# Performance work log

Measured on AMD Instinct MI355X. Metric: run time of the kernel, lower is better.

## Reference

```python
import jax, jax.numpy as jnp
import numpy as np

NUM_STREAMS = 4
DIM = 256
SINKHORN_ITERS = 10
SINKHORN_TAU = 0.05


def sinkhorn_log(logits, num_iters=SINKHORN_ITERS, tau=SINKHORN_TAU):
    n = logits.shape[-1]
    z = logits / tau
    log_marginal = -jnp.log(jnp.asarray(float(n), dtype=logits.dtype))

    def body(carry, _):
        u, v = carry
        u = log_marginal - jax.scipy.special.logsumexp(z + v[None, :], axis=1)
        v = log_marginal - jax.scipy.special.logsumexp(z + u[:, None], axis=0)
        return (u, v), None

    u0 = jnp.zeros((n,), dtype=z.dtype)
    v0 = jnp.zeros((n,), dtype=z.dtype)
    (u, v), _ = jax.lax.scan(body, (u0, v0), None, length=num_iters)
    return jnp.exp(z + u[:, None] + v[None, :]) * n


def setup_inputs() -> dict:
    key = jax.random.key(0)
    k_res, k_w = jax.random.split(key)
    B = 65536
    residuals = jax.random.normal(k_res, (B, NUM_STREAMS, DIM), dtype=jnp.float32)
    # h_res_logits: -8 everywhere, 0 on diagonal (as in __init__)
    h_res_logits = jnp.full((NUM_STREAMS, NUM_STREAMS), -8.0, dtype=jnp.float32)
    h_res_logits = h_res_logits.at[jnp.arange(NUM_STREAMS), jnp.arange(NUM_STREAMS)].set(0.0)
    # h_pre_logits: -8 everywhere, 0 at init_residual_index=0
    h_pre_logits = jnp.full((NUM_STREAMS,), -8.0, dtype=jnp.float32).at[0].set(0.0)
    h_post_logits = jnp.zeros((NUM_STREAMS,), dtype=jnp.float32)
    # branch Linear(dim, dim, bias=False): weight (out, in), y = x @ W.T
    bound = 1.0 / np.sqrt(DIM)
    W_branch = jax.random.uniform(k_w, (DIM, DIM), dtype=jnp.float32, minval=-bound, maxval=bound)
    return {
        "residuals": residuals,
        "h_res_logits": h_res_logits,
        "h_pre_logits": h_pre_logits,
        "h_post_logits": h_post_logits,
        "W_branch": W_branch,
    }


def reference(residuals, h_res_logits, h_pre_logits, h_post_logits, W_branch):
    # residuals: (B, S, D)
    h_res = sinkhorn_log(h_res_logits)                     # (S, S) doubly-stochastic * n
    h_pre = jax.nn.softmax(h_pre_logits)                   # (S,)
    h_post = jax.nn.softmax(h_post_logits)                 # (S,)
    residuals_mixed = jnp.einsum('st,bsd->btd', h_res, residuals)
    branch_input = jnp.einsum('s,bsd->bd', h_pre, residuals)
    branch_output = branch_input @ W_branch.T              # (B, D)
    depth_out = jnp.einsum('bd,s->bsd', branch_output, h_post)
    return residuals_mixed + depth_out
```

## Files before the change

kernel.cpp:

```cpp
#include <hip/hip_runtime.h>

#define NSTREAMS 4
#define DIM 256
#define BM 16
#define NTHREADS 512
#define TILES 8

typedef __attribute__((ext_vector_type(8))) short short8;
typedef __attribute__((ext_vector_type(4))) float f32x4;

static __device__ __forceinline__ short f2bf(float x) {
    union { float f; unsigned int u; } c; c.f = x;
    unsigned int u = c.u;
    unsigned int lsb = (u >> 16) & 1u;
    u += 0x7fffu + lsb;
    return (short)(u >> 16);
}
static __device__ __forceinline__ int2 f2bf4(float4 v) {
    unsigned int lo, hi;
    asm("v_cvt_pk_bf16_f32 %0, %1, %2" : "=v"(lo) : "v"(v.x), "v"(v.y));
    asm("v_cvt_pk_bf16_f32 %0, %1, %2" : "=v"(hi) : "v"(v.z), "v"(v.w));
    int2 r; r.x = (int)lo; r.y = (int)hi;
    return r;
}

static __device__ __forceinline__ float rfl(float x) {
    int i = __builtin_amdgcn_readfirstlane(__builtin_bit_cast(int, x));
    return __builtin_bit_cast(float, i);
}

static __device__ __forceinline__ void barrier_lgkm() {
    asm volatile("s_waitcnt lgkmcnt(0)\n\ts_barrier" ::: "memory");
}

static __device__ void compute_h(const float* __restrict__ hres_l,
                                 const float* __restrict__ hpre_l,
                                 const float* __restrict__ hpost_l,
                                 float* h_out) {
    const float inv_tau = 1.0f / 0.05f;
    float z[4][4];
    for (int i = 0; i < 4; ++i)
        for (int j = 0; j < 4; ++j)
            z[i][j] = hres_l[i * 4 + j] * inv_tau;
    float u[4] = {0.f, 0.f, 0.f, 0.f};
    float v[4] = {0.f, 0.f, 0.f, 0.f};
    const float logm = -logf(4.0f);
    for (int it = 0; it < 10; ++it) {
        for (int i = 0; i < 4; ++i) {
            float m = -1e30f;
            for (int j = 0; j < 4; ++j) m = fmaxf(m, z[i][j] + v[j]);
            float ss = 0.f;
            for (int j = 0; j < 4; ++j) ss += expf(z[i][j] + v[j] - m);
            u[i] = logm - (m + logf(ss));
        }
        for (int j = 0; j < 4; ++j) {
            float m = -1e30f;
            for (int i = 0; i < 4; ++i) m = fmaxf(m, z[i][j] + u[i]);
            float ss = 0.f;
            for (int i = 0; i < 4; ++i) ss += expf(z[i][j] + u[i] - m);
            v[j] = logm - (m + logf(ss));
        }
    }
    for (int i = 0; i < 4; ++i)
        for (int j = 0; j < 4; ++j)
            h_out[i * 4 + j] = expf(z[i][j] + u[i] + v[j]) * 4.0f;
    {
        float m = fmaxf(fmaxf(hpre_l[0], hpre_l[1]), fmaxf(hpre_l[2], hpre_l[3]));
        float e0 = expf(hpre_l[0] - m), e1 = expf(hpre_l[1] - m);
        float e2 = expf(hpre_l[2] - m), e3 = expf(hpre_l[3] - m);
        float ss = e0 + e1 + e2 + e3;
        h_out[16] = e0 / ss; h_out[17] = e1 / ss; h_out[18] = e2 / ss; h_out[19] = e3 / ss;
    }
    {
        float m = fmaxf(fmaxf(hpost_l[0], hpost_l[1]), fmaxf(hpost_l[2], hpost_l[3]));
        float e0 = expf(hpost_l[0] - m), e1 = expf(hpost_l[1] - m);
        float e2 = expf(hpost_l[2] - m), e3 = expf(hpost_l[3] - m);
        float ss = e0 + e1 + e2 + e3;
        h_out[20] = e0 / ss; h_out[21] = e1 / ss; h_out[22] = e2 / ss; h_out[23] = e3 / ss;
    }
}

__global__ void prep_h_kernel(const float* __restrict__ hres_l,
                              const float* __restrict__ hpre_l,
                              const float* __restrict__ hpost_l,
                              float* __restrict__ ws) {
    if (threadIdx.x == 0) compute_h(hres_l, hpre_l, hpost_l, ws);
}

__global__ __launch_bounds__(256) void prep_wh_kernel(const float* __restrict__ Wb,
                                                      short* __restrict__ wbf,
                                                      const float* __restrict__ hres_l,
                                                      const float* __restrict__ hpre_l,
                                                      const float* __restrict__ hpost_l,
                                                      float* __restrict__ ws_h) {
    int idx = blockIdx.x * 256 + threadIdx.x;
    float4 v = reinterpret_cast<const float4*>(Wb)[idx];
    reinterpret_cast<int2*>(wbf)[idx] = f2bf4(v);
    if (blockIdx.x == 0 && threadIdx.x == 0)
        compute_h(hres_l, hpre_l, hpost_l, ws_h);
}

template <bool USE_WSW>
__global__ __launch_bounds__(NTHREADS, 2) void fused_kernel(
    const float* __restrict__ res,
    const float* __restrict__ Wb,
    const short* __restrict__ wbf,
    const float* __restrict__ hptr,
    const float* __restrict__ hres_l,
    const float* __restrict__ hpre_l,
    const float* __restrict__ hpost_l,
    float* __restrict__ out)
{
    __shared__ __align__(16) short bi_lds[BM][DIM + 8];
    __shared__ __align__(16) float bo_lds[BM][DIM + 4];
    __shared__ float h_sh[24];

    const int t  = threadIdx.x;
    const int d4 = t & 63;
    const int r0 = t >> 6;
    const int w  = t >> 6;
    const int l  = t & 63;
    const int lr = l & 15;
    const int lk = l >> 4;

    if (hptr) {
        if (t < 24) h_sh[t] = hptr[t];
    } else if (t == 0) {
        compute_h(hres_l, hpre_l, hpost_l, h_sh);
    }
    barrier_lgkm();

    const float hp0 = rfl(h_sh[16]), hp1 = rfl(h_sh[17]);
    const float hp2 = rfl(h_sh[18]), hp3 = rfl(h_sh[19]);
    float hres[4][4];
    #pragma unroll
    for (int s = 0; s < 4; ++s)
        #pragma unroll
        for (int tt = 0; tt < 4; ++tt)
            hres[s][tt] = rfl(h_sh[s * 4 + tt]);
    float hq[4] = {rfl(h_sh[20]), rfl(h_sh[21]), rfl(h_sh[22]), rfl(h_sh[23])};

    const long tile0 = (long)blockIdx.x * TILES;

    float4 cur[2][4];
    #pragma unroll
    for (int it = 0; it < 2; ++it) {
        int r = r0 + it * 8;
        const float4* p = reinterpret_cast<const float4*>(
            res + (tile0 * BM + r) * (NSTREAMS * DIM)) + d4;
        cur[it][0] = p[0];
        cur[it][1] = p[64];
        cur[it][2] = p[128];
        cur[it][3] = p[192];
        float4 bi;
        bi.x = hp0 * cur[it][0].x + hp1 * cur[it][1].x + hp2 * cur[it][2].x + hp3 * cur[it][3].x;
        bi.y = hp0 * cur[it][0].y + hp1 * cur[it][1].y + hp2 * cur[it][2].y + hp3 * cur[it][3].y;
        bi.z = hp0 * cur[it][0].z + hp1 * cur[it][1].z + hp2 * cur[it][2].z + hp3 * cur[it][3].z;
        bi.w = hp0 * cur[it][0].w + hp1 * cur[it][1].w + hp2 * cur[it][2].w + hp3 * cur[it][3].w;
        *reinterpret_cast<int2*>(&bi_lds[r][d4 * 4]) = f2bf4(bi);
    }
    barrier_lgkm();

    for (int ti = 0; ti < TILES; ++ti) {
        f32x4 acc[2] = {f32x4{0.f, 0.f, 0.f, 0.f}, f32x4{0.f, 0.f, 0.f, 0.f}};
        for (int k0 = 0; k0 < DIM; k0 += 32) {
            short8 a = *reinterpret_cast<const short8*>(&bi_lds[lr][k0 + lk * 8]);
            #pragma unroll
            for (int nt = 0; nt < 2; ++nt) {
                int dcol = w * 32 + nt * 16 + lr;
                short8 b;
                if (USE_WSW) {
                    b = *reinterpret_cast<const short8*>(wbf + dcol * DIM + k0 + lk * 8);
                } else {
                    const float4* wp = reinterpret_cast<const float4*>(Wb + dcol * DIM + k0 + lk * 8);
                    float4 wa = wp[0];
                    float4 wb2 = wp[1];
                    b[0] = f2bf(wa.x); b[1] = f2bf(wa.y); b[2] = f2bf(wa.z); b[3] = f2bf(wa.w);
                    b[4] = f2bf(wb2.x); b[5] = f2bf(wb2.y); b[6] = f2bf(wb2.z); b[7] = f2bf(wb2.w);
                }
                acc[nt] = __builtin_amdgcn_mfma_f32_16x16x32_bf16(a, b, acc[nt], 0, 0, 0);
            }
        }

        float4 nx[2][4];
        const bool more = (ti + 1 < TILES);
        if (more) {
            #pragma unroll
            for (int it = 0; it < 2; ++it) {
                int r = r0 + it * 8;
                const float4* p = reinterpret_cast<const float4*>(
                    res + ((tile0 + ti + 1) * BM + r) * (NSTREAMS * DIM)) + d4;
                nx[it][0] = p[0];
                nx[it][1] = p[64];
                nx[it][2] = p[128];
                nx[it][3] = p[192];
            }
        }

        #pragma unroll
        for (int nt = 0; nt < 2; ++nt) {
            int d = w * 32 + nt * 16 + lr;
            #pragma unroll
            for (int j = 0; j < 4; ++j)
                bo_lds[lk * 4 + j][d] = acc[nt][j];
        }
        barrier_lgkm();

        #pragma unroll
        for (int it = 0; it < 2; ++it) {
            int r = r0 + it * 8;
            float4 bo = *reinterpret_cast<const float4*>(&bo_lds[r][d4 * 4]);
            float* obase = out + (((tile0 + ti) * BM + r) * 4) * DIM + d4 * 4;
            #pragma unroll
            for (int tt = 0; tt < 4; ++tt) {
                float4 o;
                o.x = hq[tt] * bo.x + hres[0][tt] * cur[it][0].x + hres[1][tt] * cur[it][1].x
                    + hres[2][tt] * cur[it][2].x + hres[3][tt] * cur[it][3].x;
                o.y = hq[tt] * bo.y + hres[0][tt] * cur[it][0].y + hres[1][tt] * cur[it][1].y
                    + hres[2][tt] * cur[it][2].y + hres[3][tt] * cur[it][3].y;
                o.z = hq[tt] * bo.z + hres[0][tt] * cur[it][0].z + hres[1][tt] * cur[it][1].z
                    + hres[2][tt] * cur[it][2].z + hres[3][tt] * cur[it][3].z;
                o.w = hq[tt] * bo.w + hres[0][tt] * cur[it][0].w + hres[1][tt] * cur[it][1].w
                    + hres[2][tt] * cur[it][2].w + hres[3][tt] * cur[it][3].w;
                *reinterpret_cast<float4*>(obase + tt * DIM) = o;
            }
        }

        if (more) {
            #pragma unroll
            for (int it = 0; it < 2; ++it) {
                int r = r0 + it * 8;
                float4 bi;
                bi.x = hp0 * nx[it][0].x + hp1 * nx[it][1].x + hp2 * nx[it][2].x + hp3 * nx[it][3].x;
                bi.y = hp0 * nx[it][0].y + hp1 * nx[it][1].y + hp2 * nx[it][2].y + hp3 * nx[it][3].y;
                bi.z = hp0 * nx[it][0].z + hp1 * nx[it][1].z + hp2 * nx[it][2].z + hp3 * nx[it][3].z;
                bi.w = hp0 * nx[it][0].w + hp1 * nx[it][1].w + hp2 * nx[it][2].w + hp3 * nx[it][3].w;
                *reinterpret_cast<int2*>(&bi_lds[r][d4 * 4]) = f2bf4(bi);
                #pragma unroll
                for (int s = 0; s < 4; ++s)
                    cur[it][s] = nx[it][s];
            }
        }
        barrier_lgkm();
    }
}

extern "C" void kernel_launch(void* const* d_in, const int* in_sizes, int n_in,
                              void* d_out, int out_size, void* d_ws, size_t ws_size,
                              hipStream_t stream) {
    const float* res     = (const float*)d_in[0];
    const float* hres_l  = (const float*)d_in[1];
    const float* hpre_l  = (const float*)d_in[2];
    const float* hpost_l = (const float*)d_in[3];
    const float* Wb      = (const float*)d_in[4];
    float* out = (float*)d_out;

    const int Btot = in_sizes[0] / (NSTREAMS * DIM);
    const int grid = Btot / (BM * TILES);

    const size_t W_OFF = 256;
    const size_t need_h = 24 * sizeof(float);
    const size_t need_w = W_OFF + (size_t)DIM * DIM * sizeof(short);
    const bool has_h = ws_size >= need_h;
    const bool has_w = ws_size >= need_w;

    float* ws_h = (float*)d_ws;
    short* ws_w = (short*)((char*)d_ws + W_OFF);

    if (has_w) {
        prep_wh_kernel<<<(DIM * DIM / 4) / 256, 256, 0, stream>>>(
            Wb, ws_w, hres_l, hpre_l, hpost_l, ws_h);
        fused_kernel<true><<<grid, NTHREADS, 0, stream>>>(
            res, Wb, ws_w, ws_h, hres_l, hpre_l, hpost_l, out);
    } else if (has_h) {
        prep_h_kernel<<<1, 64, 0, stream>>>(hres_l, hpre_l, hpost_l, ws_h);
        fused_kernel<false><<<grid, NTHREADS, 0, stream>>>(
            res, Wb, nullptr, ws_h, hres_l, hpre_l, hpost_l, out);
    } else {
        fused_kernel<false><<<grid, NTHREADS, 0, stream>>>(
            res, Wb, nullptr, nullptr, hres_l, hpre_l, hpost_l, out);
    }
}
```

Measured before the change: 129.7 us.

## Stage full bf16 weight matrix in swizzled LDS with 1024-thread blocks

The whole 256x256 bf16 branch weight is loaded once per block into an XOR-swizzled LDS buffer, so the MFMA loop no longer reads W from global or L2 on every tile. Blocks grow to 1024 threads (16 waves, one 16-column slice each) and each block now covers 16 tiles, with the next tile's residual prefetch issued before the MFMA loop. The cost is 128KB of LDS and one block per CU, which reduces occupancy. It also puts a 128KB weight load at the start of every block.

```diff
diff --git a/kernel.cpp b/kernel.cpp
--- a/kernel.cpp
+++ b/kernel.cpp
@@ -3,8 +3,8 @@
 #define NSTREAMS 4
 #define DIM 256
 #define BM 16
-#define NTHREADS 512
-#define TILES 8
+#define NTHREADS 1024
+#define TILES 16
 
 typedef __attribute__((ext_vector_type(8))) short short8;
 typedef __attribute__((ext_vector_type(4))) float f32x4;
@@ -101,7 +101,7 @@
 }
 
 template <bool USE_WSW>
-__global__ __launch_bounds__(NTHREADS, 2) void fused_kernel(
+__global__ __launch_bounds__(NTHREADS, 1) void fused_kernel(
     const float* __restrict__ res,
     const float* __restrict__ Wb,
     const short* __restrict__ wbf,
@@ -111,6 +111,7 @@
     const float* __restrict__ hpost_l,
     float* __restrict__ out)
 {
+    __shared__ __align__(16) short W_lds[DIM * DIM];
     __shared__ __align__(16) short bi_lds[BM][DIM + 8];
     __shared__ __align__(16) float bo_lds[BM][DIM + 4];
     __shared__ float h_sh[24];
@@ -122,6 +123,35 @@
     const int l  = t & 63;
     const int lr = l & 15;
     const int lk = l >> 4;
+
+    const long tile0 = (long)blockIdx.x * TILES;
+    float4 cur[4];
+    {
+        const float4* p = reinterpret_cast<const float4*>(
+            res + (tile0 * BM + r0) * (NSTREAMS * DIM)) + d4;
+        cur[0] = p[0];
+        cur[1] = p[64];
+        cur[2] = p[128];
+        cur[3] = p[192];
+    }
+
+    #pragma unroll
+    for (int i = 0; i < 8; ++i) {
+        int c = t * 8 + i;
+        int row = c >> 5;
+        int koff = (c & 31) * 16;
+        int dst = (row << 9) | (koff ^ ((row & 7) << 4));
+        int4 wv;
+        if (USE_WSW) {
+            wv = reinterpret_cast<const int4*>(wbf)[c];
+        } else {
+            const float4* wp = reinterpret_cast<const float4*>(Wb) + c * 2;
+            float4 wa = wp[0], wb2 = wp[1];
+            int2 loq = f2bf4(wa), hiq = f2bf4(wb2);
+            wv.x = loq.x; wv.y = loq.y; wv.z = hiq.x; wv.w = hiq.y;
+        }
+        *reinterpret_cast<int4*>(reinterpret_cast<char*>(W_lds) + dst) = wv;
+    }
 
     if (hptr) {
         if (t < 24) h_sh[t] = hptr[t];
@@ -140,106 +170,77 @@
             hres[s][tt] = rfl(h_sh[s * 4 + tt]);
     float hq[4] = {rfl(h_sh[20]), rfl(h_sh[21]), rfl(h_sh[22]), rfl(h_sh[23])};
 
-    const long tile0 = (long)blockIdx.x * TILES;
-
-    float4 cur[2][4];
-    #pragma unroll
-    for (int it = 0; it < 2; ++it) {
-        int r = r0 + it * 8;
-        const float4* p = reinterpret_cast<const float4*>(
-            res + (tile0 * BM + r) * (NSTREAMS * DIM)) + d4;
-        cur[it][0] = p[0];
-        cur[it][1] = p[64];
-        cur[it][2] = p[128];
-        cur[it][3] = p[192];
+    {
         float4 bi;
-        bi.x = hp0 * cur[it][0].x + hp1 * cur[it][1].x + hp2 * cur[it][2].x + hp3 * cur[it][3].x;
-        bi.y = hp0 * cur[it][0].y + hp1 * cur[it][1].y + hp2 * cur[it][2].y + hp3 * cur[it][3].y;
-        bi.z = hp0 * cur[it][0].z + hp1 * cur[it][1].z + hp2 * cur[it][2].z + hp3 * cur[it][3].z;
-        bi.w = hp0 * cur[it][0].w + hp1 * cur[it][1].w + hp2 * cur[it][2].w + hp3 * cur[it][3].w;
-        *reinterpret_cast<int2*>(&bi_lds[r][d4 * 4]) = f2bf4(bi);
+        bi.x = hp0 * cur[0].x + hp1 * cur[1].x + hp2 * cur[2].x + hp3 * cur[3].x;
+        bi.y = hp0 * cur[0].y + hp1 * cur[1].y + hp2 * cur[2].y + hp3 * cur[3].y;
+        bi.z = hp0 * cur[0].z + hp1 * cur[1].z + hp2 * cur[2].z + hp3 * cur[3].z;
+        bi.w = hp0 * cur[0].w + hp1 * cur[1].w + hp2 * cur[2].w + hp3 * cur[3].w;
+        *reinterpret_cast<int2*>(&bi_lds[r0][d4 * 4]) = f2bf4(bi);
     }
     barrier_lgkm();
 
+    const int dcol = w * 16 + lr;
+    const char* wbase = reinterpret_cast<const char*>(W_lds) + (dcol << 9);
+    const int dswz = (dcol & 7) << 4;
+
     for (int ti = 0; ti < TILES; ++ti) {
-        f32x4 acc[2] = {f32x4{0.f, 0.f, 0.f, 0.f}, f32x4{0.f, 0.f, 0.f, 0.f}};
+        const bool more = (ti + 1 < TILES);
+
+        float4 nx[4];
+        if (more) {
+            const float4* p = reinterpret_cast<const float4*>(
+                res + ((tile0 + ti + 1) * BM + r0) * (NSTREAMS * DIM)) + d4;
+            nx[0] = p[0];
+            nx[1] = p[64];
+            nx[2] = p[128];
+            nx[3] = p[192];
+        }
+        __builtin_amdgcn_sched_barrier(0);
+
+        f32x4 acc = {0.f, 0.f, 0.f, 0.f};
+        #pragma unroll
         for (int k0 = 0; k0 < DIM; k0 += 32) {
             short8 a = *reinterpret_cast<const short8*>(&bi_lds[lr][k0 + lk * 8]);
-            #pragma unroll
-            for (int nt = 0; nt < 2; ++nt) {
-                int dcol = w * 32 + nt * 16 + lr;
-                short8 b;
-                if (USE_WSW) {
-                    b = *reinterpret_cast<const short8*>(wbf + dcol * DIM + k0 + lk * 8);
-                } else {
-                    const float4* wp = reinterpret_cast<const float4*>(Wb + dcol * DIM + k0 + lk * 8);
-                    float4 wa = wp[0];
-                    float4 wb2 = wp[1];
-                    b[0] = f2bf(wa.x); b[1] = f2bf(wa.y); b[2] = f2bf(wa.z); b[3] = f2bf(wa.w);
-                    b[4] = f2bf(wb2.x); b[5] = f2bf(wb2.y); b[6] = f2bf(wb2.z); b[7] = f2bf(wb2.w);
-                }
-                acc[nt] = __builtin_amdgcn_mfma_f32_16x16x32_bf16(a, b, acc[nt], 0, 0, 0);
-            }
-        }
-
-        float4 nx[2][4];
-        const bool more = (ti + 1 < TILES);
-        if (more) {
-            #pragma unroll
-            for (int it = 0; it < 2; ++it) {
-                int r = r0 + it * 8;
-                const float4* p = reinterpret_cast<const float4*>(
-                    res + ((tile0 + ti + 1) * BM + r) * (NSTREAMS * DIM)) + d4;
-                nx[it][0] = p[0];
-                nx[it][1] = p[64];
-                nx[it][2] = p[128];
-                nx[it][3] = p[192];
-            }
+            short8 b = *reinterpret_cast<const short8*>(
+                wbase + ((k0 * 2 + lk * 16) ^ dswz));
+            acc = __builtin_amdgcn_mfma_f32_16x16x32_bf16(a, b, acc, 0, 0, 0);
         }
 
         #pragma unroll
-        for (int nt = 0; nt < 2; ++nt) {
-            int d = w * 32 + nt * 16 + lr;
-            #pragma unroll
-            for (int j = 0; j < 4; ++j)
-                bo_lds[lk * 4 + j][d] = acc[nt][j];
-        }
+        for (int j = 0; j < 4; ++j)
+            bo_lds[lk * 4 + j][dcol] = acc[j];
+
         barrier_lgkm();
 
-        #pragma unroll
-        for (int it = 0; it < 2; ++it) {
-            int r = r0 + it * 8;
-            float4 bo = *reinterpret_cast<const float4*>(&bo_lds[r][d4 * 4]);
-            float* obase = out + (((tile0 + ti) * BM + r) * 4) * DIM + d4 * 4;
+        {
+            float4 bo = *reinterpret_cast<const float4*>(&bo_lds[r0][d4 * 4]);
+            float* obase = out + (((tile0 + ti) * BM + r0) * 4) * DIM + d4 * 4;
             #pragma unroll
             for (int tt = 0; tt < 4; ++tt) {
                 float4 o;
-                o.x = hq[tt] * bo.x + hres[0][tt] * cur[it][0].x + hres[1][tt] * cur[it][1].x
-                    + hres[2][tt] * cur[it][2].x + hres[3][tt] * cur[it][3].x;
-                o.y = hq[tt] * bo.y + hres[0][tt] * cur[it][0].y + hres[1][tt] * cur[it][1].y
-                    + hres[2][tt] * cur[it][2].y + hres[3][tt] * cur[it][3].y;
-                o.z = hq[tt] * bo.z + hres[0][tt] * cur[it][0].z + hres[1][tt] * cur[it][1].z
-                    + hres[2][tt] * cur[it][2].z + hres[3][tt] * cur[it][3].z;
-                o.w = hq[tt] * bo.w + hres[0][tt] * cur[it][0].w + hres[1][tt] * cur[it][1].w
-                    + hres[2][tt] * cur[it][2].w + hres[3][tt] * cur[it][3].w;
+                o.x = hq[tt] * bo.x + hres[0][tt] * cur[0].x + hres[1][tt] * cur[1].x
+                    + hres[2][tt] * cur[2].x + hres[3][tt] * cur[3].x;
+                o.y = hq[tt] * bo.y + hres[0][tt] * cur[0].y + hres[1][tt] * cur[1].y
+                    + hres[2][tt] * cur[2].y + hres[3][tt] * cur[3].y;
+                o.z = hq[tt] * bo.z + hres[0][tt] * cur[0].z + hres[1][tt] * cur[1].z
+                    + hres[2][tt] * cur[2].z + hres[3][tt] * cur[3].z;
+                o.w = hq[tt] * bo.w + hres[0][tt] * cur[0].w + hres[1][tt] * cur[1].w
+                    + hres[2][tt] * cur[2].w + hres[3][tt] * cur[3].w;
                 *reinterpret_cast<float4*>(obase + tt * DIM) = o;
             }
         }
 
         if (more) {
+            float4 bi;
+            bi.x = hp0 * nx[0].x + hp1 * nx[1].x + hp2 * nx[2].x + hp3 * nx[3].x;
+            bi.y = hp0 * nx[0].y + hp1 * nx[1].y + hp2 * nx[2].y + hp3 * nx[3].y;
+            bi.z = hp0 * nx[0].z + hp1 * nx[1].z + hp2 * nx[2].z + hp3 * nx[3].z;
+            bi.w = hp0 * nx[0].w + hp1 * nx[1].w + hp2 * nx[2].w + hp3 * nx[3].w;
+            *reinterpret_cast<int2*>(&bi_lds[r0][d4 * 4]) = f2bf4(bi);
             #pragma unroll
-            for (int it = 0; it < 2; ++it) {
-                int r = r0 + it * 8;
-                float4 bi;
-                bi.x = hp0 * nx[it][0].x + hp1 * nx[it][1].x + hp2 * nx[it][2].x + hp3 * nx[it][3].x;
-                bi.y = hp0 * nx[it][0].y + hp1 * nx[it][1].y + hp2 * nx[it][2].y + hp3 * nx[it][3].y;
-                bi.z = hp0 * nx[it][0].z + hp1 * nx[it][1].z + hp2 * nx[it][2].z + hp3 * nx[it][3].z;
-                bi.w = hp0 * nx[it][0].w + hp1 * nx[it][1].w + hp2 * nx[it][2].w + hp3 * nx[it][3].w;
-                *reinterpret_cast<int2*>(&bi_lds[r][d4 * 4]) = f2bf4(bi);
-                #pragma unroll
-                for (int s = 0; s < 4; ++s)
-                    cur[it][s] = nx[it][s];
-            }
+            for (int s = 0; s < 4; ++s)
+                cur[s] = nx[s];
         }
         barrier_lgkm();
     }
```

Measured after the change: 128.7 us. No clear change (-0.8%).
